# Kernel tuning notes

Hardware: AMD Instinct MI355X
Metric: run time of the kernel (lower is better)

## Reference

```python
import jax, jax.numpy as jnp
import numpy as np

N_NODES = 40000

def setup_inputs() -> dict:
    key = jax.random.key(0)
    k1, k2, k3, k4 = jax.random.split(key, 4)
    x = jax.random.normal(k1, (N_NODES, 256), dtype=jnp.float32)
    edge_index = jax.random.randint(k2, (2, 640000), 0, N_NODES, dtype=jnp.int64)
    W = jax.random.normal(k3, (256, 128), dtype=jnp.float32) * (1.0 / np.sqrt(256))
    b = jax.random.normal(k4, (128,), dtype=jnp.float32) * 0.01
    return {"x": x, "edge_index": edge_index, "W": W, "b": b}

def reference(x, edge_index, W, b):
    N = x.shape[0]
    # GCNConv: add self-loops, symmetric degree normalization, linear, aggregate, bias
    loops = jnp.arange(N, dtype=edge_index.dtype)
    src = jnp.concatenate([edge_index[0], loops])  # message sources j
    dst = jnp.concatenate([edge_index[1], loops])  # targets i
    ones = jnp.ones_like(dst, dtype=x.dtype)
    deg = jax.ops.segment_sum(ones, dst, num_segments=N)  # in-degree incl. self-loop
    dinv = jnp.where(deg > 0, jax.lax.rsqrt(deg), 0.0)
    norm = dinv[src] * dinv[dst]  # [E+N]
    xw = x @ W  # transform first (in_dim -> out_dim), as in PyG GCNConv
    msgs = norm[:, None] * xw[src]  # [E+N, out_dim]
    agg = jax.ops.segment_sum(msgs, dst, num_segments=N) + b
    return jax.nn.relu(agg)  # dropout_value == 0 -> no dropout
```

## Files before the change

### kernel.cpp

```cpp
#include <hip/hip_runtime.h>

#define N_NODES 40000
#define IN_DIM 256
#define OUT_DIM 128
#define CAP 64
#define GEMM_BLOCKS 625
#define FILL_BLOCKS 625

typedef __bf16 bf16x8 __attribute__((ext_vector_type(8)));
typedef float floatx4 __attribute__((ext_vector_type(4)));

__device__ __forceinline__ int clamp_idx(int v) {
    unsigned u = (unsigned)v;
    return (u < (unsigned)N_NODES) ? v : 0;
}

__device__ __forceinline__ int ld_edge(const int* e32, long long idx, int is64) {
    return is64 ? e32[2 * idx] : e32[idx];
}

__device__ __forceinline__ float bflo(unsigned u) {
    union { unsigned i; float f; } c; c.i = u << 16; return c.f;
}
__device__ __forceinline__ float bfhi(unsigned u) {
    union { unsigned i; float f; } c; c.i = u & 0xFFFF0000u; return c.f;
}

__global__ void prep_r19(const int* __restrict__ edge32, int* __restrict__ flag,
                         int* __restrict__ cnt, const float* __restrict__ W,
                         __bf16* __restrict__ wswz) {
    int i = blockIdx.x * 256 + threadIdx.x;
    if (i < N_NODES) cnt[i] = 0;
    if (i < IN_DIM * OUT_DIM) {
        int j    = i & 7;
        int lane = (i >> 3) & 63;
        int tile = i >> 9;
        int ct = tile & 7, kc = tile >> 3;
        int k = kc * 32 + (lane >> 4) * 8 + j;
        int n = ct * 16 + (lane & 15);
        wswz[i] = (__bf16)W[k * OUT_DIM + n];
    }
    if (blockIdx.x == 0) {
        __shared__ int sh[256];
        int t = threadIdx.x;
        int nz = 0;
        for (int k = t; k < 1000; k += 256) nz |= (edge32[2 * k + 1] != 0);
        sh[t] = nz;
        __syncthreads();
        for (int off = 128; off > 0; off >>= 1) {
            if (t < off) sh[t] |= sh[t + off];
            __syncthreads();
        }
        if (t == 0) *flag = sh[0] ? 0 : 1;
    }
}

__global__ __launch_bounds__(256) void main_r19(
    const float* __restrict__ x, const __bf16* __restrict__ wswz,
    __bf16* __restrict__ xwb,
    const void* __restrict__ edge, int E, const int* __restrict__ flag,
    int* __restrict__ cnt, unsigned short* __restrict__ bucket) {
    __shared__ __align__(16) float4 wlds4[4096];
    int t = threadIdx.x;
    int bid = blockIdx.x;
    if ((bid & 1) == 0) {
        int gid = bid >> 1;
        const float4* wsrc = (const float4*)wswz;
#pragma unroll
        for (int i = 0; i < 16; ++i) wlds4[i * 256 + t] = wsrc[i * 256 + t];
        __syncthreads();

        int wave = t >> 6, lane = t & 63;
        int quad = lane >> 4, m16 = lane & 15;
        int m = gid * 64 + wave * 16 + m16;
        const float* xrow = x + (long long)m * IN_DIM;
        const char* wl = (const char*)wlds4 + (lane << 4);

        floatx4 acc[8];
#pragma unroll
        for (int ct = 0; ct < 8; ++ct) acc[ct] = (floatx4){0.f, 0.f, 0.f, 0.f};

#pragma unroll
        for (int kc = 0; kc < 8; ++kc) {
            int k0 = kc * 32 + quad * 8;
            float4 xa = *(const float4*)(xrow + k0);
            float4 xb = *(const float4*)(xrow + k0 + 4);
            bf16x8 af;
            af[0] = (__bf16)xa.x; af[1] = (__bf16)xa.y;
            af[2] = (__bf16)xa.z; af[3] = (__bf16)xa.w;
            af[4] = (__bf16)xb.x; af[5] = (__bf16)xb.y;
            af[6] = (__bf16)xb.z; af[7] = (__bf16)xb.w;
#pragma unroll
            for (int ct = 0; ct < 8; ++ct) {
                bf16x8 bf = *(const bf16x8*)(wl + ((kc * 8 + ct) << 10));
                acc[ct] = __builtin_amdgcn_mfma_f32_16x16x32_bf16(af, bf, acc[ct], 0, 0, 0);
            }
        }

        unsigned* xwu = (unsigned*)xwb;
        int rbase = gid * 64 + wave * 16 + quad * 4;
#pragma unroll
        for (int p = 0; p < 4; ++p) {
#pragma unroll
            for (int r = 0; r < 4; ++r) {
                __bf16 lo = (__bf16)acc[2 * p][r];
                __bf16 hi = (__bf16)acc[2 * p + 1][r];
                unsigned u = ((unsigned)__builtin_bit_cast(unsigned short, hi) << 16)
                           | (unsigned)__builtin_bit_cast(unsigned short, lo);
                xwu[(long long)(rbase + r) * 64 + p * 16 + m16] = u;
            }
        }
    } else {
        int is64 = *flag;
        const int* e32 = (const int*)edge;
        long long base = (long long)(bid >> 1) * 1024 + t * 4;
        int s0 = clamp_idx(ld_edge(e32, base + 0, is64));
        int s1 = clamp_idx(ld_edge(e32, base + 1, is64));
        int s2 = clamp_idx(ld_edge(e32, base + 2, is64));
        int s3 = clamp_idx(ld_edge(e32, base + 3, is64));
        int d0 = clamp_idx(ld_edge(e32, E + base + 0, is64));
        int d1 = clamp_idx(ld_edge(e32, E + base + 1, is64));
        int d2 = clamp_idx(ld_edge(e32, E + base + 2, is64));
        int d3 = clamp_idx(ld_edge(e32, E + base + 3, is64));
        int p0 = atomicAdd(&cnt[d0], 1);
        int p1 = atomicAdd(&cnt[d1], 1);
        int p2 = atomicAdd(&cnt[d2], 1);
        int p3 = atomicAdd(&cnt[d3], 1);
        if (p0 < CAP) bucket[d0 * CAP + p0] = (unsigned short)s0;
        if (p1 < CAP) bucket[d1 * CAP + p1] = (unsigned short)s1;
        if (p2 < CAP) bucket[d2 * CAP + p2] = (unsigned short)s2;
        if (p3 < CAP) bucket[d3 * CAP + p3] = (unsigned short)s3;
    }
}

__global__ void gather_r19(const unsigned short* __restrict__ bucket,
                           const int* __restrict__ cnt,
                           const unsigned* __restrict__ xwd, const float* __restrict__ b,
                           float* __restrict__ out) {
    int node = blockIdx.x * 4 + (threadIdx.x >> 6);
    int lane = threadIdx.x & 63;
    if (node >= N_NODES) return;
    int cc = (lane >> 4) * 32 + (lane & 15);
    float b0 = b[cc], b1 = b[cc + 16];
    int cn_true = cnt[node];
    int take = cn_true < CAP ? cn_true : CAP;
    float dd = rsqrtf((float)(cn_true + 1));
    unsigned us = xwd[node * 64 + lane];
    float a0 = dd * dd * bflo(us);
    float a1 = dd * dd * bfhi(us);

    int s_l = 0; float nrm_l = 0.0f;
    if (lane < take) {
        s_l = (int)bucket[node * CAP + lane];
        nrm_l = dd * rsqrtf((float)(cnt[s_l] + 1));
    }
    int j = 0;
    for (; j + 8 <= take; j += 8) {
        int   s0 = __shfl(s_l, j),     s1 = __shfl(s_l, j + 1);
        int   s2 = __shfl(s_l, j + 2), s3 = __shfl(s_l, j + 3);
        int   s4 = __shfl(s_l, j + 4), s5 = __shfl(s_l, j + 5);
        int   s6 = __shfl(s_l, j + 6), s7 = __shfl(s_l, j + 7);
        float n0 = __shfl(nrm_l, j),     n1 = __shfl(nrm_l, j + 1);
        float n2 = __shfl(nrm_l, j + 2), n3 = __shfl(nrm_l, j + 3);
        float n4 = __shfl(nrm_l, j + 4), n5 = __shfl(nrm_l, j + 5);
        float n6 = __shfl(nrm_l, j + 6), n7 = __shfl(nrm_l, j + 7);
        unsigned u0 = xwd[s0 * 64 + lane], u1 = xwd[s1 * 64 + lane];
        unsigned u2 = xwd[s2 * 64 + lane], u3 = xwd[s3 * 64 + lane];
        unsigned u4 = xwd[s4 * 64 + lane], u5 = xwd[s5 * 64 + lane];
        unsigned u6 = xwd[s6 * 64 + lane], u7 = xwd[s7 * 64 + lane];
        a0 += n0 * bflo(u0); a1 += n0 * bfhi(u0);
        a0 += n1 * bflo(u1); a1 += n1 * bfhi(u1);
        a0 += n2 * bflo(u2); a1 += n2 * bfhi(u2);
        a0 += n3 * bflo(u3); a1 += n3 * bfhi(u3);
        a0 += n4 * bflo(u4); a1 += n4 * bfhi(u4);
        a0 += n5 * bflo(u5); a1 += n5 * bfhi(u5);
        a0 += n6 * bflo(u6); a1 += n6 * bfhi(u6);
        a0 += n7 * bflo(u7); a1 += n7 * bfhi(u7);
    }
    for (; j < take; ++j) {
        int   s = __shfl(s_l, j);
        float n = __shfl(nrm_l, j);
        unsigned u = xwd[s * 64 + lane];
        a0 += n * bflo(u); a1 += n * bfhi(u);
    }
    out[(long long)node * OUT_DIM + cc]      = fmaxf(a0 + b0, 0.0f);
    out[(long long)node * OUT_DIM + cc + 16] = fmaxf(a1 + b1, 0.0f);
}

extern "C" void kernel_launch(void* const* d_in, const int* in_sizes, int n_in,
                              void* d_out, int out_size, void* d_ws, size_t ws_size,
                              hipStream_t stream) {
    const float* x   = (const float*)d_in[0];
    const void* edge = d_in[1];
    const float* W   = (const float*)d_in[2];
    const float* b   = (const float*)d_in[3];
    float* out       = (float*)d_out;

    int E = in_sizes[1] / 2;

    char* ws = (char*)d_ws;
    int*            cnt    = (int*)(ws);
    int*            flag   = (int*)(ws + 160000);
    __bf16*         wswz   = (__bf16*)(ws + 160256);
    unsigned short* bucket = (unsigned short*)(ws + 225792);
    __bf16*         xwb    = (__bf16*)(ws + 5345792);

    prep_r19<<<160, 256, 0, stream>>>((const int*)edge, flag, cnt, W, wswz);
    main_r19<<<GEMM_BLOCKS + FILL_BLOCKS, 256, 0, stream>>>(
        x, wswz, xwb, edge, E, flag, cnt, bucket);
    gather_r19<<<N_NODES / 4, 256, 0, stream>>>(bucket, cnt, (const unsigned*)xwb, b, out);
}
```

Measured before the change: 143.3 us.

## Fold prep kernel into main: in-block W swizzle, per-block dtype detect, memset

Removes the separate prep kernel. Each GEMM block now converts and swizzles W from fp32 into LDS itself, in two K-halves so the LDS footprint is halved. Each fill block detects the int32/int64 edge layout locally, and a memset zeroes the counters. This saves one kernel launch and its serialization, but every GEMM block now redundantly reads W and does scattered 2-byte LDS writes, with an extra barrier in between.

```diff
diff --git a/kernel.cpp b/kernel.cpp
--- a/kernel.cpp
+++ b/kernel.cpp
@@ -26,49 +26,17 @@
     union { unsigned i; float f; } c; c.i = u & 0xFFFF0000u; return c.f;
 }
 
-__global__ void prep_r19(const int* __restrict__ edge32, int* __restrict__ flag,
-                         int* __restrict__ cnt, const float* __restrict__ W,
-                         __bf16* __restrict__ wswz) {
-    int i = blockIdx.x * 256 + threadIdx.x;
-    if (i < N_NODES) cnt[i] = 0;
-    if (i < IN_DIM * OUT_DIM) {
-        int j    = i & 7;
-        int lane = (i >> 3) & 63;
-        int tile = i >> 9;
-        int ct = tile & 7, kc = tile >> 3;
-        int k = kc * 32 + (lane >> 4) * 8 + j;
-        int n = ct * 16 + (lane & 15);
-        wswz[i] = (__bf16)W[k * OUT_DIM + n];
-    }
-    if (blockIdx.x == 0) {
-        __shared__ int sh[256];
-        int t = threadIdx.x;
-        int nz = 0;
-        for (int k = t; k < 1000; k += 256) nz |= (edge32[2 * k + 1] != 0);
-        sh[t] = nz;
-        __syncthreads();
-        for (int off = 128; off > 0; off >>= 1) {
-            if (t < off) sh[t] |= sh[t + off];
-            __syncthreads();
-        }
-        if (t == 0) *flag = sh[0] ? 0 : 1;
-    }
-}
-
-__global__ __launch_bounds__(256) void main_r19(
-    const float* __restrict__ x, const __bf16* __restrict__ wswz,
+__global__ __launch_bounds__(256) void main_r23(
+    const float* __restrict__ x, const float* __restrict__ W,
     __bf16* __restrict__ xwb,
-    const void* __restrict__ edge, int E, const int* __restrict__ flag,
+    const void* __restrict__ edge, int E,
     int* __restrict__ cnt, unsigned short* __restrict__ bucket) {
-    __shared__ __align__(16) float4 wlds4[4096];
+    __shared__ __align__(16) float4 wlds4[2048];
     int t = threadIdx.x;
     int bid = blockIdx.x;
     if ((bid & 1) == 0) {
         int gid = bid >> 1;
-        const float4* wsrc = (const float4*)wswz;
-#pragma unroll
-        for (int i = 0; i < 16; ++i) wlds4[i * 256 + t] = wsrc[i * 256 + t];
-        __syncthreads();
+        __bf16* wb = (__bf16*)wlds4;
 
         int wave = t >> 6, lane = t & 63;
         int quad = lane >> 4, m16 = lane & 15;
@@ -76,24 +44,50 @@
         const float* xrow = x + (long long)m * IN_DIM;
         const char* wl = (const char*)wlds4 + (lane << 4);
 
+        int krow = t >> 1;
+        int c0 = (t & 1) * 64;
+
         floatx4 acc[8];
 #pragma unroll
         for (int ct = 0; ct < 8; ++ct) acc[ct] = (floatx4){0.f, 0.f, 0.f, 0.f};
 
 #pragma unroll
-        for (int kc = 0; kc < 8; ++kc) {
-            int k0 = kc * 32 + quad * 8;
-            float4 xa = *(const float4*)(xrow + k0);
-            float4 xb = *(const float4*)(xrow + k0 + 4);
-            bf16x8 af;
-            af[0] = (__bf16)xa.x; af[1] = (__bf16)xa.y;
-            af[2] = (__bf16)xa.z; af[3] = (__bf16)xa.w;
-            af[4] = (__bf16)xb.x; af[5] = (__bf16)xb.y;
-            af[6] = (__bf16)xb.z; af[7] = (__bf16)xb.w;
-#pragma unroll
-            for (int ct = 0; ct < 8; ++ct) {
-                bf16x8 bf = *(const bf16x8*)(wl + ((kc * 8 + ct) << 10));
-                acc[ct] = __builtin_amdgcn_mfma_f32_16x16x32_bf16(af, bf, acc[ct], 0, 0, 0);
+        for (int h = 0; h < 2; ++h) {
+            if (h) __syncthreads();
+            int k = h * 128 + krow;
+            int jj = k & 7;
+            int laneHi16 = ((k >> 3) & 3) * 16;
+            int tbase = ((k >> 5) - h * 4) * 8;
+            const float4* wrow4 = (const float4*)(W + (long long)k * OUT_DIM + c0);
+#pragma unroll
+            for (int f = 0; f < 16; ++f) {
+                float4 w4 = wrow4[f];
+                int n0 = c0 + 4 * f;
+#pragma unroll
+                for (int e = 0; e < 4; ++e) {
+                    int n = n0 + e;
+                    int idx = (tbase + (n >> 4)) * 512 + (laneHi16 + (n & 15)) * 8 + jj;
+                    float v = (e == 0) ? w4.x : (e == 1) ? w4.y : (e == 2) ? w4.z : w4.w;
+                    wb[idx] = (__bf16)v;
+                }
+            }
+            __syncthreads();
+#pragma unroll
+            for (int kcl = 0; kcl < 4; ++kcl) {
+                int kc = h * 4 + kcl;
+                int k0 = kc * 32 + quad * 8;
+                float4 xa = *(const float4*)(xrow + k0);
+                float4 xb = *(const float4*)(xrow + k0 + 4);
+                bf16x8 af;
+                af[0] = (__bf16)xa.x; af[1] = (__bf16)xa.y;
+                af[2] = (__bf16)xa.z; af[3] = (__bf16)xa.w;
+                af[4] = (__bf16)xb.x; af[5] = (__bf16)xb.y;
+                af[6] = (__bf16)xb.z; af[7] = (__bf16)xb.w;
+#pragma unroll
+                for (int ct = 0; ct < 8; ++ct) {
+                    bf16x8 bf = *(const bf16x8*)(wl + ((kcl * 8 + ct) << 10));
+                    acc[ct] = __builtin_amdgcn_mfma_f32_16x16x32_bf16(af, bf, acc[ct], 0, 0, 0);
+                }
             }
         }
 
@@ -111,8 +105,17 @@
             }
         }
     } else {
-        int is64 = *flag;
         const int* e32 = (const int*)edge;
+        int* sh = (int*)wlds4;
+        if (t == 0) sh[0] = 0;
+        __syncthreads();
+        int nz = 0;
+#pragma unroll
+        for (int q = 0; q < 4; ++q) nz |= e32[2 * (t * 4 + q) + 1];
+        if (nz) sh[0] = 1;
+        __syncthreads();
+        int is64 = !sh[0];
+
         long long base = (long long)(bid >> 1) * 1024 + t * 4;
         int s0 = clamp_idx(ld_edge(e32, base + 0, is64));
         int s1 = clamp_idx(ld_edge(e32, base + 1, is64));
@@ -133,7 +136,7 @@
     }
 }
 
-__global__ void gather_r19(const unsigned short* __restrict__ bucket,
+__global__ void gather_r23(const unsigned short* __restrict__ bucket,
                            const int* __restrict__ cnt,
                            const unsigned* __restrict__ xwd, const float* __restrict__ b,
                            float* __restrict__ out) {
@@ -200,13 +203,11 @@
 
     char* ws = (char*)d_ws;
     int*            cnt    = (int*)(ws);
-    int*            flag   = (int*)(ws + 160000);
-    __bf16*         wswz   = (__bf16*)(ws + 160256);
-    unsigned short* bucket = (unsigned short*)(ws + 225792);
-    __bf16*         xwb    = (__bf16*)(ws + 5345792);
-
-    prep_r19<<<160, 256, 0, stream>>>((const int*)edge, flag, cnt, W, wswz);
-    main_r19<<<GEMM_BLOCKS + FILL_BLOCKS, 256, 0, stream>>>(
-        x, wswz, xwb, edge, E, flag, cnt, bucket);
-    gather_r19<<<N_NODES / 4, 256, 0, stream>>>(bucket, cnt, (const unsigned*)xwb, b, out);
-}
+    unsigned short* bucket = (unsigned short*)(ws + 160000);
+    __bf16*         xwb    = (__bf16*)(ws + 5280000);
+
+    hipMemsetAsync(cnt, 0, N_NODES * sizeof(int), stream);
+    main_r23<<<GEMM_BLOCKS + FILL_BLOCKS, 256, 0, stream>>>(
+        x, W, xwb, edge, E, cnt, bucket);
+    gather_r23<<<N_NODES / 4, 256, 0, stream>>>(bucket, cnt, (const unsigned*)xwb, b, out);
+}
```

Result: slower. 155.9 us (+8.8%).
